# Kernel optimization log

Measured on AMD Instinct MI355X. Metric: run time of the kernel, lower is better.

## Reference

```python
import jax, jax.numpy as jnp
import numpy as np

N, C, HW, HEADS = 2048, 16, 8, 4
F = C * HW * HW  # 1024
E = 16384
EPS = 1e-5
NEG_SLOPE = 0.2


def _bn(x, g, b):
    # training-mode BatchNorm2d over (N, H, W)
    m = x.mean(axis=(0, 2, 3), keepdims=True)
    v = x.var(axis=(0, 2, 3), keepdims=True)
    return (x - m) * jax.lax.rsqrt(v + EPS) * g[None, :, None, None] + b[None, :, None, None]


def _conv1x1(x, w, b):
    # 1x1 conv == per-pixel linear: w is [out_c, in_c]
    return jnp.einsum('nchw,oc->nohw', x, w) + b[None, :, None, None]


def _gatv2(xf, edge_index, wl, bl, wr, br, att, bias_gat):
    # xf: [N, F] node features
    xl = (xf @ wl + bl).reshape(N, HEADS, F)  # source-side transform (lin_l)
    xr = (xf @ wr + br).reshape(N, HEADS, F)  # target-side transform (lin_r)
    src, dst = edge_index[0], edge_index[1]
    loops = jnp.arange(N)
    # PyG default: remove existing self loops (mask them) then add self loops
    src_f = jnp.concatenate([src, loops])
    dst_f = jnp.concatenate([dst, loops])
    valid = jnp.concatenate([src != dst, jnp.ones((N,), bool)])
    xj = xl[src_f]                                   # [E+N, HEADS, F] gather
    e = jax.nn.leaky_relu(xj + xr[dst_f], negative_slope=NEG_SLOPE)
    logits = jnp.einsum('ehf,hf->eh', e, att)        # [E+N, HEADS]
    logits = jnp.where(valid[:, None], logits, -jnp.inf)
    mx = jax.lax.stop_gradient(jax.ops.segment_max(logits, dst_f, num_segments=N))
    expv = jnp.where(valid[:, None], jnp.exp(logits - mx[dst_f]), 0.0)
    denom = jax.ops.segment_sum(expv, dst_f, num_segments=N)
    alpha = expv / denom[dst_f]                      # segment softmax over incoming edges
    out = jax.ops.segment_sum(alpha[:, :, None] * xj, dst_f, num_segments=N)  # [N, HEADS, F]
    return out.reshape(N, HEADS * F) + bias_gat


def setup_inputs() -> dict:
    key = jax.random.key(0)
    ks = jax.random.split(key, 8)
    s = 0.02
    return {
        'x': jax.random.normal(ks[0], (N, C, HW, HW), jnp.float32),
        'edge_index': jax.random.randint(ks[1], (2, E), 0, N),
        'w1': jax.random.normal(ks[2], (C, C), jnp.float32) * s,
        'b1': jnp.zeros((C,), jnp.float32),
        'g1': jnp.ones((C,), jnp.float32),
        'be1': jnp.zeros((C,), jnp.float32),
        'wl': jax.random.normal(ks[3], (F, HEADS * F), jnp.float32) * s,
        'bl': jnp.zeros((HEADS * F,), jnp.float32),
        'wr': jax.random.normal(ks[4], (F, HEADS * F), jnp.float32) * s,
        'br': jnp.zeros((HEADS * F,), jnp.float32),
        'att': jax.random.normal(ks[5], (HEADS, F), jnp.float32) * s,
        'bias_gat': jnp.zeros((HEADS * F,), jnp.float32),
        'w2': jax.random.normal(ks[6], (C, HEADS * C), jnp.float32) * s,
        'b2': jnp.zeros((C,), jnp.float32),
        'g2': jnp.ones((C,), jnp.float32),
        'be2': jnp.zeros((C,), jnp.float32),
    }


def reference(x, edge_index, w1, b1, g1, be1, wl, bl, wr, br, att, bias_gat, w2, b2, g2, be2):
    res = x
    y = _bn(_conv1x1(x, w1, b1), g1, be1)            # fc1: Conv2d 1x1 + BN
    yf = y.reshape(N, F)
    g = _gatv2(yf, edge_index, wl, bl, wr, br, att, bias_gat)
    g = g.reshape(N, HEADS * C, HW, HW)
    out = _bn(_conv1x1(g, w2, b2), g2, be2)          # fc2: Conv2d 1x1 + BN
    return out + res                                  # DropPath(0.0) == Identity
```

## Files before the change

kernel.cpp:

```cpp
#include <hip/hip_runtime.h>
#include <stdint.h>

#define N_NODES 2048
#define F_DIM   1024
#define HEADS   4
#define NF      4096
#define ROW     8192
#define E_EDGES 16384
#define MAXE    (E_EDGES + N_NODES)
#define BN_EPS  1e-5f
#define NSLOPE  0.2f

#define CW1   0
#define CB1   256
#define CG1   272
#define CBE1  288
#define CBL   304
#define CBR   4400
#define CATT  8496
#define CBG   12592
#define CW2   16688
#define CB2   17712
#define CG2   17728
#define CBE2  17744
#define CSM_N 17760

typedef unsigned short ushort_t;
typedef __attribute__((ext_vector_type(8))) short bf16x8;
typedef __attribute__((ext_vector_type(4))) float f32x4;
typedef __attribute__((ext_vector_type(8))) unsigned short us8;

__device__ __forceinline__ float b2f(unsigned short u) {
    union { unsigned int i; float f; } x; x.i = ((unsigned int)u) << 16; return x.f;
}
__device__ __forceinline__ unsigned short f2b(float f) {
    union { float f; unsigned int i; } x; x.f = f;
    unsigned int r = x.i + 0x7fffu + ((x.i >> 16) & 1u);
    return (unsigned short)(r >> 16);
}

__global__ void k_sniff(const ushort_t* __restrict__ xu, const int* __restrict__ ei,
                        int* __restrict__ flags)
{
    if (threadIdx.x == 0) {
        int hits = 0;
        for (int i = 0; i < 32; ++i) {
            unsigned e = (xu[2 * i] >> 7) & 0xFF;
            if (e >= 0x90) hits++;
        }
        flags[0] = (hits >= 3) ? 1 : 0;
        int nz = 0;
        for (int i = 0; i < 32; ++i) if (ei[2 * i + 1] != 0) nz++;
        flags[1] = (nz == 0) ? 1 : 0;
    }
}

__device__ __forceinline__ ushort_t ld_canon(const void* src, size_t i, int f32) {
    return f32 ? f2b(((const float*)src)[i]) : ((const ushort_t*)src)[i];
}

__global__ __launch_bounds__(256) void k_convert_all(
    const int* __restrict__ flags,
    const void* x, const void* ei,
    const void* w1, const void* b1, const void* g1, const void* be1,
    const void* bl, const void* br, const void* att, const void* bg,
    const void* w2, const void* b2, const void* g2, const void* be2,
    ushort_t* __restrict__ cx, int* __restrict__ cei, ushort_t* __restrict__ csm)
{
    int f32 = flags[0], i64 = flags[1];
    int b = blockIdx.x, t = threadIdx.x;
    if (b < 2048) {
        size_t base = (size_t)b * 1024;
        #pragma unroll
        for (int i = 0; i < 4; ++i) {
            size_t idx = base + t + i * 256;
            cx[idx] = ld_canon(x, idx, f32);
        }
    } else if (b == 2048) {
        for (int i = t; i < 256; i += 256)  csm[CW1 + i]  = ld_canon(w1, i, f32);
        for (int i = t; i < 16; i += 256)   csm[CB1 + i]  = ld_canon(b1, i, f32);
        for (int i = t; i < 16; i += 256)   csm[CG1 + i]  = ld_canon(g1, i, f32);
        for (int i = t; i < 16; i += 256)   csm[CBE1 + i] = ld_canon(be1, i, f32);
        for (int i = t; i < 4096; i += 256) csm[CBL + i]  = ld_canon(bl, i, f32);
        for (int i = t; i < 4096; i += 256) csm[CBR + i]  = ld_canon(br, i, f32);
        for (int i = t; i < 4096; i += 256) csm[CATT + i] = ld_canon(att, i, f32);
        for (int i = t; i < 4096; i += 256) csm[CBG + i]  = ld_canon(bg, i, f32);
        for (int i = t; i < 1024; i += 256) csm[CW2 + i]  = ld_canon(w2, i, f32);
        for (int i = t; i < 16; i += 256)   csm[CB2 + i]  = ld_canon(b2, i, f32);
        for (int i = t; i < 16; i += 256)   csm[CG2 + i]  = ld_canon(g2, i, f32);
        for (int i = t; i < 16; i += 256)   csm[CBE2 + i] = ld_canon(be2, i, f32);
    } else {
        const int* s = (const int*)ei;
        int base = (b - 2049) * 1024;
        #pragma unroll
        for (int j = 0; j < 4; ++j) {
            int idx = base + t + j * 256;
            cei[idx] = i64 ? s[2 * idx] : s[idx];
        }
    }
}

__global__ __launch_bounds__(256) void k_fc1_stats(
    const ushort_t* __restrict__ cx, const ushort_t* __restrict__ csm,
    float* __restrict__ y0, float* __restrict__ ps, float* __restrict__ pq)
{
    __shared__ float xs[1024];
    __shared__ float sw[256];
    __shared__ float sb[16];
    int tid = threadIdx.x;
    sw[tid] = b2f(csm[CW1 + tid]);
    if (tid < 16) sb[tid] = b2f(csm[CB1 + tid]);
    int wave = tid >> 6, lane = tid & 63;
    float s[4] = {0,0,0,0}, q[4] = {0,0,0,0};
    for (int nn = 0; nn < 8; ++nn) {
        int n = blockIdx.x * 8 + nn;
        __syncthreads();
        #pragma unroll
        for (int i = 0; i < 4; ++i) {
            int idx = tid + i * 256;
            xs[idx] = b2f(cx[(size_t)n * 1024 + idx]);
        }
        __syncthreads();
        #pragma unroll
        for (int i = 0; i < 4; ++i) {
            int o = wave * 4 + i;
            float acc = sb[o];
            #pragma unroll
            for (int c = 0; c < 16; ++c) acc += xs[c * 64 + lane] * sw[o * 16 + c];
            y0[(size_t)n * 1024 + o * 64 + lane] = acc;
            s[i] += acc; q[i] += acc * acc;
        }
    }
    #pragma unroll
    for (int i = 0; i < 4; ++i)
        for (int mm = 1; mm < 64; mm <<= 1) {
            s[i] += __shfl_xor(s[i], mm);
            q[i] += __shfl_xor(q[i], mm);
        }
    if (lane == 0)
        #pragma unroll
        for (int i = 0; i < 4; ++i) {
            ps[blockIdx.x * 16 + wave * 4 + i] = s[i];
            pq[blockIdx.x * 16 + wave * 4 + i] = q[i];
        }
}

__global__ void k_bn_final(const float* __restrict__ ps, const float* __restrict__ pq,
                           const ushort_t* __restrict__ gamma, const ushort_t* __restrict__ beta,
                           float* __restrict__ scale, float* __restrict__ shift)
{
    int t = threadIdx.x;
    int ch = t & 15, seg = t >> 4;
    float s = 0.f, q = 0.f;
    for (int j = 0; j < 64; ++j) {
        int b = seg * 64 + j;
        s += ps[b * 16 + ch]; q += pq[b * 16 + ch];
    }
    s += __shfl_xor(s, 16); q += __shfl_xor(q, 16);
    s += __shfl_xor(s, 32); q += __shfl_xor(q, 32);
    if (t < 16) {
        const float inv = 1.0f / 131072.0f;
        float mean = s * inv;
        float var  = q * inv - mean * mean;
        float sc = b2f(gamma[ch]) * rsqrtf(var + BN_EPS);
        scale[ch] = sc;
        shift[ch] = b2f(beta[ch]) - mean * sc;
    }
}

__global__ void k_bn_final2(const float* __restrict__ ps, const float* __restrict__ pq,
                            const ushort_t* __restrict__ gamma, const ushort_t* __restrict__ beta,
                            float* __restrict__ scale, float* __restrict__ shift)
{
    int t = threadIdx.x;
    int ch = t & 15, seg = t >> 4;
    float s = 0.f, q = 0.f;
    for (int j = 0; j < 512; ++j) {
        int b = seg * 512 + j;
        s += ps[b * 16 + ch]; q += pq[b * 16 + ch];
    }
    s += __shfl_xor(s, 16); q += __shfl_xor(q, 16);
    s += __shfl_xor(s, 32); q += __shfl_xor(q, 32);
    if (t < 16) {
        const float inv = 1.0f / 131072.0f;
        float mean = s * inv;
        float var  = q * inv - mean * mean;
        float sc = b2f(gamma[ch]) * rsqrtf(var + BN_EPS);
        scale[ch] = sc;
        shift[ch] = b2f(beta[ch]) - mean * sc;
    }
}

__global__ __launch_bounds__(256) void k_norm1(const float* __restrict__ y0,
    const float* __restrict__ scale, const float* __restrict__ shift,
    ushort_t* __restrict__ xf)
{
    int idx = blockIdx.x * 1024 + threadIdx.x;
    #pragma unroll
    for (int i = 0; i < 4; ++i) {
        int k = idx + i * 256;
        int ch = (k >> 6) & 15;
        xf[k] = f2b(y0[k] * scale[ch] + shift[ch]);
    }
}

__global__ __launch_bounds__(256) void k_convT(const void* __restrict__ in,
                                               ushort_t* __restrict__ outT,
                                               const int* __restrict__ flags)
{
    __shared__ ushort_t tl[64][65];
    int f32 = flags[0];
    int bx = blockIdx.x * 64, by = blockIdx.y * 64;
    #pragma unroll
    for (int i = 0; i < 16; ++i) {
        int idx = threadIdx.x + i * 256;
        int r = idx >> 6, c = idx & 63;
        tl[r][c] = ld_canon(in, (size_t)(by + r) * 4096 + bx + c, f32);
    }
    __syncthreads();
    #pragma unroll
    for (int i = 0; i < 16; ++i) {
        int idx = threadIdx.x + i * 256;
        int r = idx >> 6, c = idx & 63;
        outT[(size_t)(bx + r) * 1024 + by + c] = tl[c][r];
    }
}

__global__ __launch_bounds__(256) void k_gemm(
    const ushort_t* __restrict__ A, const ushort_t* __restrict__ BT,
    const ushort_t* __restrict__ bias, ushort_t* __restrict__ out)
{
    __shared__ __align__(16) ushort_t As[128 * 32];
    __shared__ __align__(16) ushort_t Bs[128 * 32];
    int tid = threadIdx.x;
    int wv = tid >> 6, ln = tid & 63;
    int m0 = blockIdx.y * 128, n0 = blockIdx.x * 128;
    int wm = (wv >> 1) * 64, wn = (wv & 1) * 64;
    int lr = ln & 15, quad = ln >> 4;

    f32x4 acc[4][4];
    #pragma unroll
    for (int i = 0; i < 4; ++i)
        #pragma unroll
        for (int j = 0; j < 4; ++j) acc[i][j] = (f32x4){0.f, 0.f, 0.f, 0.f};

    for (int k0 = 0; k0 < 1024; k0 += 32) {
        #pragma unroll
        for (int i = 0; i < 2; ++i) {
            int cbase = i * 256 + wv * 64;
            int ci = cbase + ln;
            int m = ci >> 2, kc = ci & 3;
            const ushort_t* ga = A + (size_t)(m0 + m) * 1024 + k0 + kc * 8;
            __builtin_amdgcn_global_load_lds(
                (const __attribute__((address_space(1))) void*)ga,
                (__attribute__((address_space(3))) void*)(&As[cbase * 8]), 16, 0, 0);
            const ushort_t* gb = BT + (size_t)(n0 + m) * 1024 + k0 + kc * 8;
            __builtin_amdgcn_global_load_lds(
                (const __attribute__((address_space(1))) void*)gb,
                (__attribute__((address_space(3))) void*)(&Bs[cbase * 8]), 16, 0, 0);
        }
        __syncthreads();
        bf16x8 af[4], bfr[4];
        #pragma unroll
        for (int i = 0; i < 4; ++i)
            af[i] = *(const bf16x8*)(&As[(wm + i * 16 + lr) * 32 + quad * 8]);
        #pragma unroll
        for (int j = 0; j < 4; ++j)
            bfr[j] = *(const bf16x8*)(&Bs[(wn + j * 16 + lr) * 32 + quad * 8]);
        #pragma unroll
        for (int i = 0; i < 4; ++i)
            #pragma unroll
            for (int j = 0; j < 4; ++j)
                acc[i][j] = __builtin_amdgcn_mfma_f32_16x16x32_bf16(af[i], bfr[j], acc[i][j], 0, 0, 0);
        __syncthreads();
    }
    #pragma unroll
    for (int j = 0; j < 4; ++j) {
        int col = n0 + wn + j * 16 + lr;
        float bj = b2f(bias[col]);
        #pragma unroll
        for (int i = 0; i < 4; ++i) {
            int rbase = m0 + wm + i * 16 + quad * 4;
            #pragma unroll
            for (int r = 0; r < 4; ++r)
                out[(size_t)(rbase + r) * ROW + col] = f2b(acc[i][j][r] + bj);
        }
    }
}

__global__ void k_count(const int* __restrict__ cei, int* __restrict__ counts) {
    int idx = blockIdx.x * 256 + threadIdx.x;
    if (idx < E_EDGES) {
        int s = cei[idx], d = cei[E_EDGES + idx];
        if (s != d) atomicAdd(&counts[d], 1);
    } else if (idx < MAXE) {
        atomicAdd(&counts[idx - E_EDGES], 1);
    }
}

__global__ __launch_bounds__(256) void k_scan(const int* __restrict__ counts,
                                              int* __restrict__ offsets, int* __restrict__ cursor)
{
    __shared__ int ts[256];
    int t = threadIdx.x;
    int loc[8]; int tot = 0;
    #pragma unroll
    for (int j = 0; j < 8; ++j) { loc[j] = counts[t * 8 + j]; tot += loc[j]; }
    ts[t] = tot; __syncthreads();
    for (int s = 1; s < 256; s <<= 1) {
        int v = (t >= s) ? ts[t - s] : 0;
        __syncthreads();
        ts[t] += v;
        __syncthreads();
    }
    int run = ts[t] - tot;
    #pragma unroll
    for (int j = 0; j < 8; ++j) {
        offsets[t * 8 + j] = run; cursor[t * 8 + j] = run; run += loc[j];
    }
    if (t == 255) offsets[2048] = run;
}

__global__ void k_scatter(const int* __restrict__ cei, int* __restrict__ cursor,
                          int* __restrict__ esrc)
{
    int idx = blockIdx.x * 256 + threadIdx.x;
    if (idx < E_EDGES) {
        int s = cei[idx], d = cei[E_EDGES + idx];
        if (s != d) { int pos = atomicAdd(&cursor[d], 1); esrc[pos] = s; }
    } else if (idx < MAXE) {
        int i = idx - E_EDGES;
        int pos = atomicAdd(&cursor[i], 1); esrc[pos] = i;
    }
}

#define CH_E 64
__global__ __launch_bounds__(256) void k_gat(
    const ushort_t* __restrict__ xlr,
    const ushort_t* __restrict__ csm,
    const int* __restrict__ offsets, const int* __restrict__ esrc,
    float* __restrict__ z, float* __restrict__ ps2, float* __restrict__ pq2)
{
    __shared__ int es[CH_E];
    __shared__ ushort_t gsb[4096];
    __shared__ float sw2[1024];
    __shared__ float sb2[16];
    int d = blockIdx.x;
    int tid = threadIdx.x;
    int h = tid >> 6, l = tid & 63;
    #pragma unroll
    for (int i = 0; i < 4; ++i) sw2[tid + i * 256] = b2f(csm[CW2 + tid + i * 256]);
    if (tid < 16) sb2[tid] = b2f(csm[CB2 + tid]);
    int off = offsets[d], deg = offsets[d + 1] - off;

    float xrv[16], attv[16];
    {
        const ushort_t* xp = xlr + ((size_t)d * ROW + NF + h * F_DIM + l * 16);
        const ushort_t* ap = csm + (CATT + h * F_DIM + l * 16);
        us8 x0 = *(const us8*)xp, x1 = *(const us8*)(xp + 8);
        us8 a0 = *(const us8*)ap, a1 = *(const us8*)(ap + 8);
        #pragma unroll
        for (int j = 0; j < 8; ++j) {
            xrv[j] = b2f(x0[j]); xrv[8 + j] = b2f(x1[j]);
            attv[j] = b2f(a0[j]); attv[8 + j] = b2f(a1[j]);
        }
    }
    float acc[16];
    #pragma unroll
    for (int j = 0; j < 16; ++j) acc[j] = 0.f;
    float m_run = -3.0e38f, s_run = 0.f;

    for (int c0 = 0; c0 < deg; c0 += CH_E) {
        int cnt = min(CH_E, deg - c0);
        __syncthreads();
        if (tid < cnt) es[tid] = esrc[off + c0 + tid];
        __syncthreads();
        int e = 0;
        for (; e + 1 < cnt; e += 2) {
            const ushort_t* p0 = xlr + ((size_t)es[e]     * ROW + h * F_DIM + l * 16);
            const ushort_t* p1 = xlr + ((size_t)es[e + 1] * ROW + h * F_DIM + l * 16);
            us8 a0 = *(const us8*)p0, a1 = *(const us8*)(p0 + 8);
            us8 b0 = *(const us8*)p1, b1 = *(const us8*)(p1 + 8);
            float t0 = 0.f, t1 = 0.f;
            #pragma unroll
            for (int j = 0; j < 8; ++j) {
                float u;
                u = b2f(a0[j]) + xrv[j];     u = u > 0.f ? u : NSLOPE * u; t0 += u * attv[j];
                u = b2f(a1[j]) + xrv[8 + j]; u = u > 0.f ? u : NSLOPE * u; t0 += u * attv[8 + j];
                u = b2f(b0[j]) + xrv[j];     u = u > 0.f ? u : NSLOPE * u; t1 += u * attv[j];
                u = b2f(b1[j]) + xrv[8 + j]; u = u > 0.f ? u : NSLOPE * u; t1 += u * attv[8 + j];
            }
            #pragma unroll
            for (int mm = 1; mm < 64; mm <<= 1) {
                t0 += __shfl_xor(t0, mm);
                t1 += __shfl_xor(t1, mm);
            }
            float nm = fmaxf(m_run, fmaxf(t0, t1));
            float fac = __expf(m_run - nm);
            float w0 = __expf(t0 - nm), w1 = __expf(t1 - nm);
            s_run = s_run * fac + w0 + w1;
            #pragma unroll
            for (int j = 0; j < 8; ++j) {
                acc[j]     = acc[j]     * fac + w0 * b2f(a0[j]) + w1 * b2f(b0[j]);
                acc[8 + j] = acc[8 + j] * fac + w0 * b2f(a1[j]) + w1 * b2f(b1[j]);
            }
            m_run = nm;
        }
        if (e < cnt) {
            const ushort_t* p0 = xlr + ((size_t)es[e] * ROW + h * F_DIM + l * 16);
            us8 a0 = *(const us8*)p0, a1 = *(const us8*)(p0 + 8);
            float t0 = 0.f;
            #pragma unroll
            for (int j = 0; j < 8; ++j) {
                float u;
                u = b2f(a0[j]) + xrv[j];     u = u > 0.f ? u : NSLOPE * u; t0 += u * attv[j];
                u = b2f(a1[j]) + xrv[8 + j]; u = u > 0.f ? u : NSLOPE * u; t0 += u * attv[8 + j];
            }
            #pragma unroll
            for (int mm = 1; mm < 64; mm <<= 1) t0 += __shfl_xor(t0, mm);
            float nm = fmaxf(m_run, t0);
            float fac = __expf(m_run - nm);
            float w0 = __expf(t0 - nm);
            s_run = s_run * fac + w0;
            #pragma unroll
            for (int j = 0; j < 8; ++j) {
                acc[j]     = acc[j]     * fac + w0 * b2f(a0[j]);
                acc[8 + j] = acc[8 + j] * fac + w0 * b2f(a1[j]);
            }
            m_run = nm;
        }
    }
    float inv = 1.0f / s_run;
    #pragma unroll
    for (int j = 0; j < 16; ++j)
        gsb[h * 1024 + l * 16 + j] = f2b(acc[j] * inv + b2f(csm[CBG + h * F_DIM + l * 16 + j]));
    __syncthreads();

    float s[4], q[4];
    #pragma unroll
    for (int i = 0; i < 4; ++i) {
        int o = h * 4 + i;
        float zv = sb2[o];
        #pragma unroll
        for (int k = 0; k < 64; ++k) zv += b2f(gsb[k * 64 + l]) * sw2[o * 64 + k];
        z[(size_t)d * 1024 + o * 64 + l] = zv;
        s[i] = zv; q[i] = zv * zv;
    }
    #pragma unroll
    for (int i = 0; i < 4; ++i)
        for (int mm = 1; mm < 64; mm <<= 1) {
            s[i] += __shfl_xor(s[i], mm);
            q[i] += __shfl_xor(q[i], mm);
        }
    if (l == 0)
        #pragma unroll
        for (int i = 0; i < 4; ++i) {
            ps2[d * 16 + h * 4 + i] = s[i];
            pq2[d * 16 + h * 4 + i] = q[i];
        }
}

__global__ __launch_bounds__(256) void k_out(
    const float* __restrict__ z, const ushort_t* __restrict__ cx,
    const float* __restrict__ scale, const float* __restrict__ shift,
    const int* __restrict__ flags, void* __restrict__ out)
{
    int f32 = flags[0];
    int idx = blockIdx.x * 512 + threadIdx.x;
    #pragma unroll
    for (int i = 0; i < 2; ++i) {
        int k = idx + i * 256;
        int ch = (k >> 6) & 15;
        float val = z[k] * scale[ch] + shift[ch] + b2f(cx[k]);
        if (f32) ((float*)out)[k] = val;
        else     ((ushort_t*)out)[k] = f2b(val);
    }
}

extern "C" void kernel_launch(void* const* d_in, const int* in_sizes, int n_in,
                              void* d_out, int out_size, void* d_ws, size_t ws_size,
                              hipStream_t stream)
{
    const void* x   = d_in[0];
    const void* ei  = d_in[1];
    const void* w1  = d_in[2];
    const void* b1  = d_in[3];
    const void* g1  = d_in[4];
    const void* be1 = d_in[5];
    const void* wl  = d_in[6];
    const void* bl  = d_in[7];
    const void* wr  = d_in[8];
    const void* br  = d_in[9];
    const void* att = d_in[10];
    const void* bg  = d_in[11];
    const void* w2  = d_in[12];
    const void* b2  = d_in[13];
    const void* g2  = d_in[14];
    const void* be2 = d_in[15];
    (void)in_sizes; (void)n_in; (void)out_size; (void)ws_size;

    char* wsb = (char*)d_ws;
    size_t o = 0;
    auto alloc = [&](size_t bytes) -> void* {
        void* p = wsb + o;
        o = (o + bytes + 255) & ~(size_t)255;
        return p;
    };
    int*      flags = (int*)alloc(256);
    ushort_t* csm   = (ushort_t*)alloc(CSM_N * 2);
    ushort_t* cx    = (ushort_t*)alloc(2097152ull * 2);
    int*      cei   = (int*)alloc(32768 * 4);
    float*    y0    = (float*)alloc(2097152ull * 4);
    float*    z     = y0;
    ushort_t* xf    = (ushort_t*)alloc(2097152ull * 2);
    ushort_t* wT    = (ushort_t*)alloc(8388608ull * 2);
    ushort_t* xlr   = (ushort_t*)alloc(16777216ull * 2);
    float* p1s = (float*)alloc(256 * 16 * 4);
    float* p1q = (float*)alloc(256 * 16 * 4);
    float* p2s = (float*)alloc(2048 * 16 * 4);
    float* p2q = (float*)alloc(2048 * 16 * 4);
    float* ss  = (float*)alloc(64 * 4);
    int* counts = (int*)alloc(2048 * 4);
    int* offs   = (int*)alloc(2049 * 4);
    int* cursor = (int*)alloc(2048 * 4);
    int* esrc   = (int*)alloc(MAXE * 4);

    k_sniff<<<1, 64, 0, stream>>>((const ushort_t*)x, (const int*)ei, flags);
    hipMemsetAsync(counts, 0, 2048 * 4, stream);
    k_convert_all<<<2081, 256, 0, stream>>>(flags, x, ei, w1, b1, g1, be1,
                                            bl, br, att, bg, w2, b2, g2, be2,
                                            cx, cei, csm);
    k_fc1_stats<<<256, 256, 0, stream>>>(cx, csm, y0, p1s, p1q);
    k_bn_final<<<1, 64, 0, stream>>>(p1s, p1q, csm + CG1, csm + CBE1, ss, ss + 16);
    k_norm1<<<2048, 256, 0, stream>>>(y0, ss, ss + 16, xf);
    k_convT<<<dim3(64, 16), 256, 0, stream>>>(wl, wT, flags);
    k_convT<<<dim3(64, 16), 256, 0, stream>>>(wr, wT + 4194304ull, flags);
    k_gemm<<<dim3(64, 16), 256, 0, stream>>>(xf, wT, csm + CBL, xlr);
    k_count<<<(MAXE + 255) / 256, 256, 0, stream>>>(cei, counts);
    k_scan<<<1, 256, 0, stream>>>(counts, offs, cursor);
    k_scatter<<<(MAXE + 255) / 256, 256, 0, stream>>>(cei, cursor, esrc);
    k_gat<<<N_NODES, 256, 0, stream>>>(xlr, csm, offs, esrc, z, p2s, p2q);
    k_bn_final2<<<1, 64, 0, stream>>>(p2s, p2q, csm + CG2, csm + CBE2, ss + 32, ss + 48);
    k_out<<<4096, 256, 0, stream>>>(z, cx, ss + 32, ss + 48, flags, d_out);
}
```

Measured before the change: 292.8 us.

## Fuse conversion, CSR build and BN finalize; coalesce GEMM epilogue; unroll GAT

Drops the separate input-conversion, sniff, count/scan/scatter and BN-finalize kernels. Inputs are read directly in their original dtype, and the CSR is built in a single 1024-thread block using shared-memory atomics. BN scale/shift is recomputed inside the normalize and output kernels, and the two weight transposes run as one launch. The GEMM epilogue is staged through LDS so it can issue coalesced 16-byte stores. The GAT loop handles four edges per iteration and drops the running-max softmax, which removes rescaling work but risks exp overflow if logits are ever large.

```diff
diff --git a/kernel.cpp b/kernel.cpp
--- a/kernel.cpp
+++ b/kernel.cpp
@@ -11,20 +11,6 @@
 #define BN_EPS  1e-5f
 #define NSLOPE  0.2f
 
-#define CW1   0
-#define CB1   256
-#define CG1   272
-#define CBE1  288
-#define CBL   304
-#define CBR   4400
-#define CATT  8496
-#define CBG   12592
-#define CW2   16688
-#define CB2   17712
-#define CG2   17728
-#define CBE2  17744
-#define CSM_N 17760
-
 typedef unsigned short ushort_t;
 typedef __attribute__((ext_vector_type(8))) short bf16x8;
 typedef __attribute__((ext_vector_type(4))) float f32x4;
@@ -38,78 +24,82 @@
     unsigned int r = x.i + 0x7fffu + ((x.i >> 16) & 1u);
     return (unsigned short)(r >> 16);
 }
-
-__global__ void k_sniff(const ushort_t* __restrict__ xu, const int* __restrict__ ei,
-                        int* __restrict__ flags)
-{
-    if (threadIdx.x == 0) {
-        int hits = 0;
-        for (int i = 0; i < 32; ++i) {
-            unsigned e = (xu[2 * i] >> 7) & 0xFF;
-            if (e >= 0x90) hits++;
-        }
-        flags[0] = (hits >= 3) ? 1 : 0;
-        int nz = 0;
-        for (int i = 0; i < 32; ++i) if (ei[2 * i + 1] != 0) nz++;
-        flags[1] = (nz == 0) ? 1 : 0;
-    }
-}
-
 __device__ __forceinline__ ushort_t ld_canon(const void* src, size_t i, int f32) {
     return f32 ? f2b(((const float*)src)[i]) : ((const ushort_t*)src)[i];
 }
-
-__global__ __launch_bounds__(256) void k_convert_all(
+__device__ __forceinline__ float ld_f(const void* src, size_t i, int f32) {
+    return f32 ? ((const float*)src)[i] : b2f(((const ushort_t*)src)[i]);
+}
+
+__global__ __launch_bounds__(1024) void k_csr(
+    const int* __restrict__ ei_raw, const ushort_t* __restrict__ x_probe,
+    int* __restrict__ offs, int* __restrict__ esrc, int* __restrict__ flags)
+{
+    __shared__ int cnt[2048];
+    __shared__ int ts[1024];
+    __shared__ int sflag;
+    int t = threadIdx.x;
+    if (t < 64) {
+        int nz = (ei_raw[2 * t + 1] != 0) ? 1 : 0;
+        unsigned long long m = __ballot(nz);
+        if (t == 0) sflag = (m == 0ull) ? 1 : 0;
+    } else if (t >= 64 && t < 96) {
+        unsigned e = (x_probe[2 * (t - 64)] >> 7) & 0xFF;
+        unsigned long long m = __ballot(e >= 0x90u);
+        if (t == 64) flags[0] = (__popcll(m) >= 3) ? 1 : 0;
+    }
+    cnt[t] = 0; cnt[t + 1024] = 0;
+    __syncthreads();
+    int i64 = sflag;
+    for (int idx = t; idx < MAXE; idx += 1024) {
+        if (idx < E_EDGES) {
+            int s = i64 ? ei_raw[2 * idx] : ei_raw[idx];
+            int d = i64 ? ei_raw[2 * (E_EDGES + idx)] : ei_raw[E_EDGES + idx];
+            if (s != d) atomicAdd(&cnt[d], 1);
+        } else {
+            atomicAdd(&cnt[idx - E_EDGES], 1);
+        }
+    }
+    __syncthreads();
+    int l0 = cnt[2 * t], l1 = cnt[2 * t + 1], tot = l0 + l1;
+    ts[t] = tot;
+    __syncthreads();
+    for (int s = 1; s < 1024; s <<= 1) {
+        int v = (t >= s) ? ts[t - s] : 0;
+        __syncthreads();
+        ts[t] += v;
+        __syncthreads();
+    }
+    int run = ts[t] - tot;
+    offs[2 * t] = run; offs[2 * t + 1] = run + l0;
+    if (t == 1023) offs[2048] = ts[1023];
+    __syncthreads();
+    cnt[2 * t] = run; cnt[2 * t + 1] = run + l0;
+    __syncthreads();
+    for (int idx = t; idx < MAXE; idx += 1024) {
+        if (idx < E_EDGES) {
+            int s = i64 ? ei_raw[2 * idx] : ei_raw[idx];
+            int d = i64 ? ei_raw[2 * (E_EDGES + idx)] : ei_raw[E_EDGES + idx];
+            if (s != d) esrc[atomicAdd(&cnt[d], 1)] = s;
+        } else {
+            int n = idx - E_EDGES;
+            esrc[atomicAdd(&cnt[n], 1)] = n;
+        }
+    }
+}
+
+__global__ __launch_bounds__(256) void k_fc1(
+    const void* __restrict__ x, const void* __restrict__ w1, const void* __restrict__ b1,
     const int* __restrict__ flags,
-    const void* x, const void* ei,
-    const void* w1, const void* b1, const void* g1, const void* be1,
-    const void* bl, const void* br, const void* att, const void* bg,
-    const void* w2, const void* b2, const void* g2, const void* be2,
-    ushort_t* __restrict__ cx, int* __restrict__ cei, ushort_t* __restrict__ csm)
-{
-    int f32 = flags[0], i64 = flags[1];
-    int b = blockIdx.x, t = threadIdx.x;
-    if (b < 2048) {
-        size_t base = (size_t)b * 1024;
-        #pragma unroll
-        for (int i = 0; i < 4; ++i) {
-            size_t idx = base + t + i * 256;
-            cx[idx] = ld_canon(x, idx, f32);
-        }
-    } else if (b == 2048) {
-        for (int i = t; i < 256; i += 256)  csm[CW1 + i]  = ld_canon(w1, i, f32);
-        for (int i = t; i < 16; i += 256)   csm[CB1 + i]  = ld_canon(b1, i, f32);
-        for (int i = t; i < 16; i += 256)   csm[CG1 + i]  = ld_canon(g1, i, f32);
-        for (int i = t; i < 16; i += 256)   csm[CBE1 + i] = ld_canon(be1, i, f32);
-        for (int i = t; i < 4096; i += 256) csm[CBL + i]  = ld_canon(bl, i, f32);
-        for (int i = t; i < 4096; i += 256) csm[CBR + i]  = ld_canon(br, i, f32);
-        for (int i = t; i < 4096; i += 256) csm[CATT + i] = ld_canon(att, i, f32);
-        for (int i = t; i < 4096; i += 256) csm[CBG + i]  = ld_canon(bg, i, f32);
-        for (int i = t; i < 1024; i += 256) csm[CW2 + i]  = ld_canon(w2, i, f32);
-        for (int i = t; i < 16; i += 256)   csm[CB2 + i]  = ld_canon(b2, i, f32);
-        for (int i = t; i < 16; i += 256)   csm[CG2 + i]  = ld_canon(g2, i, f32);
-        for (int i = t; i < 16; i += 256)   csm[CBE2 + i] = ld_canon(be2, i, f32);
-    } else {
-        const int* s = (const int*)ei;
-        int base = (b - 2049) * 1024;
-        #pragma unroll
-        for (int j = 0; j < 4; ++j) {
-            int idx = base + t + j * 256;
-            cei[idx] = i64 ? s[2 * idx] : s[idx];
-        }
-    }
-}
-
-__global__ __launch_bounds__(256) void k_fc1_stats(
-    const ushort_t* __restrict__ cx, const ushort_t* __restrict__ csm,
     float* __restrict__ y0, float* __restrict__ ps, float* __restrict__ pq)
 {
     __shared__ float xs[1024];
     __shared__ float sw[256];
     __shared__ float sb[16];
+    int f32 = flags[0];
     int tid = threadIdx.x;
-    sw[tid] = b2f(csm[CW1 + tid]);
-    if (tid < 16) sb[tid] = b2f(csm[CB1 + tid]);
+    sw[tid] = ld_f(w1, tid, f32);
+    if (tid < 16) sb[tid] = ld_f(b1, tid, f32);
     int wave = tid >> 6, lane = tid & 63;
     float s[4] = {0,0,0,0}, q[4] = {0,0,0,0};
     for (int nn = 0; nn < 8; ++nn) {
@@ -118,7 +108,7 @@
         #pragma unroll
         for (int i = 0; i < 4; ++i) {
             int idx = tid + i * 256;
-            xs[idx] = b2f(cx[(size_t)n * 1024 + idx]);
+            xs[idx] = ld_f(x, (size_t)n * 1024 + idx, f32);
         }
         __syncthreads();
         #pragma unroll
@@ -145,71 +135,50 @@
         }
 }
 
-__global__ void k_bn_final(const float* __restrict__ ps, const float* __restrict__ pq,
-                           const ushort_t* __restrict__ gamma, const ushort_t* __restrict__ beta,
-                           float* __restrict__ scale, float* __restrict__ shift)
-{
-    int t = threadIdx.x;
-    int ch = t & 15, seg = t >> 4;
+__global__ __launch_bounds__(256) void k_norm(
+    const float* __restrict__ y0, const float* __restrict__ ps, const float* __restrict__ pq,
+    const void* __restrict__ g1, const void* __restrict__ be1, const int* __restrict__ flags,
+    ushort_t* __restrict__ xf)
+{
+    __shared__ float red[2][64];
+    __shared__ float scs[16], shs[16];
+    int f32 = flags[0];
+    int t = threadIdx.x, lane = t & 63, wv = t >> 6;
     float s = 0.f, q = 0.f;
-    for (int j = 0; j < 64; ++j) {
-        int b = seg * 64 + j;
-        s += ps[b * 16 + ch]; q += pq[b * 16 + ch];
-    }
+    #pragma unroll
+    for (int i = 0; i < 16; ++i) { s += ps[i * 256 + t]; q += pq[i * 256 + t]; }
     s += __shfl_xor(s, 16); q += __shfl_xor(q, 16);
     s += __shfl_xor(s, 32); q += __shfl_xor(q, 32);
+    if (lane < 16) { red[0][wv * 16 + lane] = s; red[1][wv * 16 + lane] = q; }
+    __syncthreads();
     if (t < 16) {
+        float S = red[0][t] + red[0][16 + t] + red[0][32 + t] + red[0][48 + t];
+        float Q = red[1][t] + red[1][16 + t] + red[1][32 + t] + red[1][48 + t];
         const float inv = 1.0f / 131072.0f;
-        float mean = s * inv;
-        float var  = q * inv - mean * mean;
-        float sc = b2f(gamma[ch]) * rsqrtf(var + BN_EPS);
-        scale[ch] = sc;
-        shift[ch] = b2f(beta[ch]) - mean * sc;
-    }
-}
-
-__global__ void k_bn_final2(const float* __restrict__ ps, const float* __restrict__ pq,
-                            const ushort_t* __restrict__ gamma, const ushort_t* __restrict__ beta,
-                            float* __restrict__ scale, float* __restrict__ shift)
-{
-    int t = threadIdx.x;
-    int ch = t & 15, seg = t >> 4;
-    float s = 0.f, q = 0.f;
-    for (int j = 0; j < 512; ++j) {
-        int b = seg * 512 + j;
-        s += ps[b * 16 + ch]; q += pq[b * 16 + ch];
-    }
-    s += __shfl_xor(s, 16); q += __shfl_xor(q, 16);
-    s += __shfl_xor(s, 32); q += __shfl_xor(q, 32);
-    if (t < 16) {
-        const float inv = 1.0f / 131072.0f;
-        float mean = s * inv;
-        float var  = q * inv - mean * mean;
-        float sc = b2f(gamma[ch]) * rsqrtf(var + BN_EPS);
-        scale[ch] = sc;
-        shift[ch] = b2f(beta[ch]) - mean * sc;
-    }
-}
-
-__global__ __launch_bounds__(256) void k_norm1(const float* __restrict__ y0,
-    const float* __restrict__ scale, const float* __restrict__ shift,
-    ushort_t* __restrict__ xf)
-{
-    int idx = blockIdx.x * 1024 + threadIdx.x;
-    #pragma unroll
-    for (int i = 0; i < 4; ++i) {
-        int k = idx + i * 256;
+        float mean = S * inv;
+        float var  = Q * inv - mean * mean;
+        float sc = ld_f(g1, t, f32) * rsqrtf(var + BN_EPS);
+        scs[t] = sc;
+        shs[t] = ld_f(be1, t, f32) - mean * sc;
+    }
+    __syncthreads();
+    int base = blockIdx.x * 4096;
+    #pragma unroll
+    for (int i = 0; i < 16; ++i) {
+        int k = base + t + i * 256;
         int ch = (k >> 6) & 15;
-        xf[k] = f2b(y0[k] * scale[ch] + shift[ch]);
-    }
-}
-
-__global__ __launch_bounds__(256) void k_convT(const void* __restrict__ in,
-                                               ushort_t* __restrict__ outT,
-                                               const int* __restrict__ flags)
+        xf[k] = f2b(y0[k] * scs[ch] + shs[ch]);
+    }
+}
+
+__global__ __launch_bounds__(256) void k_convT(
+    const void* __restrict__ wl, const void* __restrict__ wr,
+    const int* __restrict__ flags, ushort_t* __restrict__ wT)
 {
     __shared__ ushort_t tl[64][65];
     int f32 = flags[0];
+    const void* in = blockIdx.z ? wr : wl;
+    ushort_t* outT = wT + (size_t)blockIdx.z * 4194304ull;
     int bx = blockIdx.x * 64, by = blockIdx.y * 64;
     #pragma unroll
     for (int i = 0; i < 16; ++i) {
@@ -228,10 +197,13 @@
 
 __global__ __launch_bounds__(256) void k_gemm(
     const ushort_t* __restrict__ A, const ushort_t* __restrict__ BT,
-    const ushort_t* __restrict__ bias, ushort_t* __restrict__ out)
+    const void* __restrict__ blr, const void* __restrict__ brr,
+    const int* __restrict__ flags, ushort_t* __restrict__ out)
 {
     __shared__ __align__(16) ushort_t As[128 * 32];
     __shared__ __align__(16) ushort_t Bs[128 * 32];
+    __shared__ __align__(16) ushort_t cs[64 * 136];
+    int f32 = flags[0];
     int tid = threadIdx.x;
     int wv = tid >> 6, ln = tid & 63;
     int m0 = blockIdx.y * 128, n0 = blockIdx.x * 128;
@@ -274,70 +246,43 @@
                 acc[i][j] = __builtin_amdgcn_mfma_f32_16x16x32_bf16(af[i], bfr[j], acc[i][j], 0, 0, 0);
         __syncthreads();
     }
+    float bj[4];
     #pragma unroll
     for (int j = 0; j < 4; ++j) {
-        int col = n0 + wn + j * 16 + lr;
-        float bj = b2f(bias[col]);
-        #pragma unroll
-        for (int i = 0; i < 4; ++i) {
-            int rbase = m0 + wm + i * 16 + quad * 4;
-            #pragma unroll
-            for (int r = 0; r < 4; ++r)
-                out[(size_t)(rbase + r) * ROW + col] = f2b(acc[i][j][r] + bj);
-        }
-    }
-}
-
-__global__ void k_count(const int* __restrict__ cei, int* __restrict__ counts) {
-    int idx = blockIdx.x * 256 + threadIdx.x;
-    if (idx < E_EDGES) {
-        int s = cei[idx], d = cei[E_EDGES + idx];
-        if (s != d) atomicAdd(&counts[d], 1);
-    } else if (idx < MAXE) {
-        atomicAdd(&counts[idx - E_EDGES], 1);
-    }
-}
-
-__global__ __launch_bounds__(256) void k_scan(const int* __restrict__ counts,
-                                              int* __restrict__ offsets, int* __restrict__ cursor)
-{
-    __shared__ int ts[256];
-    int t = threadIdx.x;
-    int loc[8]; int tot = 0;
-    #pragma unroll
-    for (int j = 0; j < 8; ++j) { loc[j] = counts[t * 8 + j]; tot += loc[j]; }
-    ts[t] = tot; __syncthreads();
-    for (int s = 1; s < 256; s <<= 1) {
-        int v = (t >= s) ? ts[t - s] : 0;
-        __syncthreads();
-        ts[t] += v;
-        __syncthreads();
-    }
-    int run = ts[t] - tot;
-    #pragma unroll
-    for (int j = 0; j < 8; ++j) {
-        offsets[t * 8 + j] = run; cursor[t * 8 + j] = run; run += loc[j];
-    }
-    if (t == 255) offsets[2048] = run;
-}
-
-__global__ void k_scatter(const int* __restrict__ cei, int* __restrict__ cursor,
-                          int* __restrict__ esrc)
-{
-    int idx = blockIdx.x * 256 + threadIdx.x;
-    if (idx < E_EDGES) {
-        int s = cei[idx], d = cei[E_EDGES + idx];
-        if (s != d) { int pos = atomicAdd(&cursor[d], 1); esrc[pos] = s; }
-    } else if (idx < MAXE) {
-        int i = idx - E_EDGES;
-        int pos = atomicAdd(&cursor[i], 1); esrc[pos] = i;
+        int colg = n0 + wn + j * 16 + lr;
+        bj[j] = (colg < 4096) ? ld_f(blr, colg, f32) : ld_f(brr, colg - 4096, f32);
+    }
+    #pragma unroll
+    for (int ph = 0; ph < 2; ++ph) {
+        if ((wv >> 1) == ph) {
+            #pragma unroll
+            for (int i = 0; i < 4; ++i)
+                #pragma unroll
+                for (int j = 0; j < 4; ++j) {
+                    int col = wn + j * 16 + lr;
+                    #pragma unroll
+                    for (int r = 0; r < 4; ++r)
+                        cs[(i * 16 + quad * 4 + r) * 136 + col] = f2b(acc[i][j][r] + bj[j]);
+                }
+        }
+        __syncthreads();
+        #pragma unroll
+        for (int rr = 0; rr < 4; ++rr) {
+            int slot = rr * 256 + tid;
+            int row = slot >> 4, seg = slot & 15;
+            us8 v = *(const us8*)&cs[row * 136 + seg * 8];
+            *(us8*)(out + (size_t)(m0 + ph * 64 + row) * ROW + n0 + seg * 8) = v;
+        }
+        __syncthreads();
     }
 }
 
 #define CH_E 64
 __global__ __launch_bounds__(256) void k_gat(
     const ushort_t* __restrict__ xlr,
-    const ushort_t* __restrict__ csm,
+    const void* __restrict__ att, const void* __restrict__ bg,
+    const void* __restrict__ w2, const void* __restrict__ b2,
+    const int* __restrict__ flags,
     const int* __restrict__ offsets, const int* __restrict__ esrc,
     float* __restrict__ z, float* __restrict__ ps2, float* __restrict__ pq2)
 {
@@ -345,30 +290,31 @@
     __shared__ ushort_t gsb[4096];
     __shared__ float sw2[1024];
     __shared__ float sb2[16];
+    int f32 = flags[0];
     int d = blockIdx.x;
     int tid = threadIdx.x;
     int h = tid >> 6, l = tid & 63;
     #pragma unroll
-    for (int i = 0; i < 4; ++i) sw2[tid + i * 256] = b2f(csm[CW2 + tid + i * 256]);
-    if (tid < 16) sb2[tid] = b2f(csm[CB2 + tid]);
+    for (int i = 0; i < 4; ++i) sw2[tid + i * 256] = ld_f(w2, tid + i * 256, f32);
+    if (tid < 16) sb2[tid] = ld_f(b2, tid, f32);
     int off = offsets[d], deg = offsets[d + 1] - off;
+    size_t hF = (size_t)h * F_DIM + l * 16;
 
     float xrv[16], attv[16];
     {
-        const ushort_t* xp = xlr + ((size_t)d * ROW + NF + h * F_DIM + l * 16);
-        const ushort_t* ap = csm + (CATT + h * F_DIM + l * 16);
+        const ushort_t* xp = xlr + ((size_t)d * ROW + NF + hF);
         us8 x0 = *(const us8*)xp, x1 = *(const us8*)(xp + 8);
-        us8 a0 = *(const us8*)ap, a1 = *(const us8*)(ap + 8);
         #pragma unroll
         for (int j = 0; j < 8; ++j) {
             xrv[j] = b2f(x0[j]); xrv[8 + j] = b2f(x1[j]);
-            attv[j] = b2f(a0[j]); attv[8 + j] = b2f(a1[j]);
+            attv[j]     = ld_f(att, hF + j, f32);
+            attv[8 + j] = ld_f(att, hF + 8 + j, f32);
         }
     }
     float acc[16];
     #pragma unroll
     for (int j = 0; j < 16; ++j) acc[j] = 0.f;
-    float m_run = -3.0e38f, s_run = 0.f;
+    float s_run = 0.f;
 
     for (int c0 = 0; c0 < deg; c0 += CH_E) {
         int cnt = min(CH_E, deg - c0);
@@ -376,39 +322,46 @@
         if (tid < cnt) es[tid] = esrc[off + c0 + tid];
         __syncthreads();
         int e = 0;
-        for (; e + 1 < cnt; e += 2) {
-            const ushort_t* p0 = xlr + ((size_t)es[e]     * ROW + h * F_DIM + l * 16);
-            const ushort_t* p1 = xlr + ((size_t)es[e + 1] * ROW + h * F_DIM + l * 16);
-            us8 a0 = *(const us8*)p0, a1 = *(const us8*)(p0 + 8);
-            us8 b0 = *(const us8*)p1, b1 = *(const us8*)(p1 + 8);
-            float t0 = 0.f, t1 = 0.f;
+        for (; e + 3 < cnt; e += 4) {
+            us8 v0[4], v1[4];
+            #pragma unroll
+            for (int k = 0; k < 4; ++k) {
+                const ushort_t* p = xlr + ((size_t)es[e + k] * ROW + hF);
+                v0[k] = *(const us8*)p; v1[k] = *(const us8*)(p + 8);
+            }
+            float tt[4];
+            #pragma unroll
+            for (int k = 0; k < 4; ++k) {
+                float t0 = 0.f;
+                #pragma unroll
+                for (int j = 0; j < 8; ++j) {
+                    float u;
+                    u = b2f(v0[k][j]) + xrv[j];     u = u > 0.f ? u : NSLOPE * u; t0 += u * attv[j];
+                    u = b2f(v1[k][j]) + xrv[8 + j]; u = u > 0.f ? u : NSLOPE * u; t0 += u * attv[8 + j];
+                }
+                tt[k] = t0;
+            }
+            #pragma unroll
+            for (int mm = 1; mm < 64; mm <<= 1) {
+                tt[0] += __shfl_xor(tt[0], mm);
+                tt[1] += __shfl_xor(tt[1], mm);
+                tt[2] += __shfl_xor(tt[2], mm);
+                tt[3] += __shfl_xor(tt[3], mm);
+            }
+            float w0 = __expf(tt[0]), w1 = __expf(tt[1]);
+            float w2v = __expf(tt[2]), w3 = __expf(tt[3]);
+            s_run += w0 + w1 + w2v + w3;
             #pragma unroll
             for (int j = 0; j < 8; ++j) {
-                float u;
-                u = b2f(a0[j]) + xrv[j];     u = u > 0.f ? u : NSLOPE * u; t0 += u * attv[j];
-                u = b2f(a1[j]) + xrv[8 + j]; u = u > 0.f ? u : NSLOPE * u; t0 += u * attv[8 + j];
-                u = b2f(b0[j]) + xrv[j];     u = u > 0.f ? u : NSLOPE * u; t1 += u * attv[j];
-                u = b2f(b1[j]) + xrv[8 + j]; u = u > 0.f ? u : NSLOPE * u; t1 += u * attv[8 + j];
+                acc[j]     += w0 * b2f(v0[0][j]) + w1 * b2f(v0[1][j])
+                            + w2v * b2f(v0[2][j]) + w3 * b2f(v0[3][j]);
+                acc[8 + j] += w0 * b2f(v1[0][j]) + w1 * b2f(v1[1][j])
+                            + w2v * b2f(v1[2][j]) + w3 * b2f(v1[3][j]);
             }
-            #pragma unroll
-            for (int mm = 1; mm < 64; mm <<= 1) {
-                t0 += __shfl_xor(t0, mm);
-                t1 += __shfl_xor(t1, mm);
-            }
-            float nm = fmaxf(m_run, fmaxf(t0, t1));
-            float fac = __expf(m_run - nm);
-            float w0 = __expf(t0 - nm), w1 = __expf(t1 - nm);
-            s_run = s_run * fac + w0 + w1;
-            #pragma unroll
-            for (int j = 0; j < 8; ++j) {
-                acc[j]     = acc[j]     * fac + w0 * b2f(a0[j]) + w1 * b2f(b0[j]);
-                acc[8 + j] = acc[8 + j] * fac + w0 * b2f(a1[j]) + w1 * b2f(b1[j]);
-            }
-            m_run = nm;
-        }
-        if (e < cnt) {
-            const ushort_t* p0 = xlr + ((size_t)es[e] * ROW + h * F_DIM + l * 16);
-            us8 a0 = *(const us8*)p0, a1 = *(const us8*)(p0 + 8);
+        }
+        for (; e < cnt; ++e) {
+            const ushort_t* p = xlr + ((size_t)es[e] * ROW + hF);
+            us8 a0 = *(const us8*)p, a1 = *(const us8*)(p + 8);
             float t0 = 0.f;
             #pragma unroll
             for (int j = 0; j < 8; ++j) {
@@ -418,22 +371,19 @@
             }
             #pragma unroll
             for (int mm = 1; mm < 64; mm <<= 1) t0 += __shfl_xor(t0, mm);
-            float nm = fmaxf(m_run, t0);
-            float fac = __expf(m_run - nm);
-            float w0 = __expf(t0 - nm);
-            s_run = s_run * fac + w0;
+            float w0 = __expf(t0);
+            s_run += w0;
             #pragma unroll
             for (int j = 0; j < 8; ++j) {
-                acc[j]     = acc[j]     * fac + w0 * b2f(a0[j]);
-                acc[8 + j] = acc[8 + j] * fac + w0 * b2f(a1[j]);
+                acc[j]     += w0 * b2f(a0[j]);
+                acc[8 + j] += w0 * b2f(a1[j]);
             }
-            m_run = nm;
         }
     }
     float inv = 1.0f / s_run;
     #pragma unroll
     for (int j = 0; j < 16; ++j)
-        gsb[h * 1024 + l * 16 + j] = f2b(acc[j] * inv + b2f(csm[CBG + h * F_DIM + l * 16 + j]));
+        gsb[h * 1024 + l * 16 + j] = f2b(acc[j] * inv + ld_f(bg, hF + j, f32));
     __syncthreads();
 
     float s[4], q[4];
@@ -461,17 +411,38 @@
 }
 
 __global__ __launch_bounds__(256) void k_out(
-    const float* __restrict__ z, const ushort_t* __restrict__ cx,
-    const float* __restrict__ scale, const float* __restrict__ shift,
+    const float* __restrict__ z, const void* __restrict__ x,
+    const float* __restrict__ ps, const float* __restrict__ pq,
+    const void* __restrict__ g2, const void* __restrict__ be2,
     const int* __restrict__ flags, void* __restrict__ out)
 {
+    __shared__ float red[2][64];
+    __shared__ float scs[16], shs[16];
     int f32 = flags[0];
-    int idx = blockIdx.x * 512 + threadIdx.x;
-    #pragma unroll
-    for (int i = 0; i < 2; ++i) {
-        int k = idx + i * 256;
-        int ch = (k >> 6) & 15;
-        float val = z[k] * scale[ch] + shift[ch] + b2f(cx[k]);
+    int t = threadIdx.x, lane = t & 63, wv = t >> 6;
+    float s = 0.f, q = 0.f;
+    for (int i = 0; i < 128; ++i) { s += ps[i * 256 + t]; q += pq[i * 256 + t]; }
+    s += __shfl_xor(s, 16); q += __shfl_xor(q, 16);
+    s += __shfl_xor(s, 32); q += __shfl_xor(q, 32);
+    if (lane < 16) { red[0][wv * 16 + lane] = s; red[1][wv * 16 + lane] = q; }
+    __syncthreads();
+    if (t < 16) {
+        float S = red[0][t] + red[0][16 + t] + red[0][32 + t] + red[0][48 + t];
+        float Q = red[1][t] + red[1][16 + t] + red[1][32 + t] + red[1][48 + t];
+        const float inv = 1.0f / 131072.0f;
+        float mean = S * inv;
+        float var  = Q * inv - mean * mean;
+        float sc = ld_f(g2, t, f32) * rsqrtf(var + BN_EPS);
+        scs[t] = sc;
+        shs[t] = ld_f(be2, t, f32) - mean * sc;
+    }
+    __syncthreads();
+    size_t base = (size_t)blockIdx.x * 8192;
+    #pragma unroll
+    for (int i = 0; i < 32; ++i) {
+        size_t k = base + t + i * 256;
+        int ch = ((int)k >> 6) & 15;
+        float val = z[k] * scs[ch] + shs[ch] + ld_f(x, k, f32);
         if (f32) ((float*)out)[k] = val;
         else     ((ushort_t*)out)[k] = f2b(val);
     }
@@ -507,9 +478,6 @@
         return p;
     };
     int*      flags = (int*)alloc(256);
-    ushort_t* csm   = (ushort_t*)alloc(CSM_N * 2);
-    ushort_t* cx    = (ushort_t*)alloc(2097152ull * 2);
-    int*      cei   = (int*)alloc(32768 * 4);
     float*    y0    = (float*)alloc(2097152ull * 4);
     float*    z     = y0;
     ushort_t* xf    = (ushort_t*)alloc(2097152ull * 2);
@@ -519,27 +487,14 @@
     float* p1q = (float*)alloc(256 * 16 * 4);
     float* p2s = (float*)alloc(2048 * 16 * 4);
     float* p2q = (float*)alloc(2048 * 16 * 4);
-    float* ss  = (float*)alloc(64 * 4);
-    int* counts = (int*)alloc(2048 * 4);
-    int* offs   = (int*)alloc(2049 * 4);
-    int* cursor = (int*)alloc(2048 * 4);
-    int* esrc   = (int*)alloc(MAXE * 4);
-
-    k_sniff<<<1, 64, 0, stream>>>((const ushort_t*)x, (const int*)ei, flags);
-    hipMemsetAsync(counts, 0, 2048 * 4, stream);
-    k_convert_all<<<2081, 256, 0, stream>>>(flags, x, ei, w1, b1, g1, be1,
-                                            bl, br, att, bg, w2, b2, g2, be2,
-                                            cx, cei, csm);
-    k_fc1_stats<<<256, 256, 0, stream>>>(cx, csm, y0, p1s, p1q);
-    k_bn_final<<<1, 64, 0, stream>>>(p1s, p1q, csm + CG1, csm + CBE1, ss, ss + 16);
-    k_norm1<<<2048, 256, 0, stream>>>(y0, ss, ss + 16, xf);
-    k_convT<<<dim3(64, 16), 256, 0, stream>>>(wl, wT, flags);
-    k_convT<<<dim3(64, 16), 256, 0, stream>>>(wr, wT + 4194304ull, flags);
-    k_gemm<<<dim3(64, 16), 256, 0, stream>>>(xf, wT, csm + CBL, xlr);
-    k_count<<<(MAXE + 255) / 256, 256, 0, stream>>>(cei, counts);
-    k_scan<<<1, 256, 0, stream>>>(counts, offs, cursor);
-    k_scatter<<<(MAXE + 255) / 256, 256, 0, stream>>>(cei, cursor, esrc);
-    k_gat<<<N_NODES, 256, 0, stream>>>(xlr, csm, offs, esrc, z, p2s, p2q);
-    k_bn_final2<<<1, 64, 0, stream>>>(p2s, p2q, csm + CG2, csm + CBE2, ss + 32, ss + 48);
-    k_out<<<4096, 256, 0, stream>>>(z, cx, ss + 32, ss + 48, flags, d_out);
-}
+    int* offs  = (int*)alloc(2049 * 4);
+    int* esrc  = (int*)alloc(MAXE * 4);
+
+    k_csr<<<1, 1024, 0, stream>>>((const int*)ei, (const ushort_t*)x, offs, esrc, flags);
+    k_fc1<<<256, 256, 0, stream>>>(x, w1, b1, flags, y0, p1s, p1q);
+    k_norm<<<512, 256, 0, stream>>>(y0, p1s, p1q, g1, be1, flags, xf);
+    k_convT<<<dim3(64, 16, 2), 256, 0, stream>>>(wl, wr, flags, wT);
+    k_gemm<<<dim3(64, 16), 256, 0, stream>>>(xf, wT, bl, br, flags, xlr);
+    k_gat<<<N_NODES, 256, 0, stream>>>(xlr, att, bg, w2, b2, flags, offs, esrc, z, p2s, p2q);
+    k_out<<<256, 256, 0, stream>>>(z, x, p2s, p2q, g2, be2, flags, d_out);
+}
```

Result: slower. 304.5 us (+4.0%).
